# Kernel tuning notes

Hardware: AMD Instinct MI355X
Metric: run time of the kernel (lower is better)

## Reference

```python
import jax, jax.numpy as jnp
import numpy as np
from jax import lax


def setup_inputs() -> dict:
    key = jax.random.key(0)
    k1, k2 = jax.random.split(key)
    x = jax.random.normal(k1, (16, 256, 64, 64), dtype=jnp.float32)
    weight = jax.random.normal(k2, (1024, 256), dtype=jnp.float32)  # codebook (K, C)
    return {"x": x, "weight": weight}


def reference(x, weight):
    B, C, H, W = x.shape
    # (b c h w) -> (b h w) c
    xf = jnp.transpose(x, (0, 2, 3, 1)).reshape(-1, C)  # [N, C]
    d = (jnp.sum(xf * xf, axis=1, keepdims=True)
         + jnp.sum(weight * weight, axis=1)
         - 2.0 * (xf @ weight.T))
    indices = jnp.argmin(d, axis=1)  # [N], int
    z = weight[indices]  # [N, C] embedding lookup
    codebook_loss = jnp.mean((z - lax.stop_gradient(xf)) ** 2)
    commitment_loss = jnp.mean((xf - lax.stop_gradient(z)) ** 2)
    # straight-through estimator
    zq = xf + lax.stop_gradient(z - xf)
    zq = zq.reshape(B, H, W, C).transpose(0, 3, 1, 2)  # back to [B, C, H, W]
    sequence = indices.reshape(B, H, W)
    return zq, sequence, codebook_loss, commitment_loss
```

## Files before the change

### kernel.cpp

```cpp
#include <hip/hip_runtime.h>
#include <cfloat>

#define B_   16
#define C_   256
#define K_   1024
#define HW_  4096
#define N_   (B_ * HW_)
#define CHW_ (C_ * HW_)

#define SEQ_OFF  (B_ * C_ * HW_)
#define LOSS_OFF (SEQ_OFF + N_)

#define WT_F    0
#define WN_F    262144
#define WHB_F   263168
#define WLB_F   394240
#define RLIST_F 525312
#define RCNT_F  590848

#define EPS_GAP 0.03125f

typedef short bf16x8 __attribute__((ext_vector_type(8)));
typedef float f32x4  __attribute__((ext_vector_type(4)));

__device__ __forceinline__ unsigned short bf16_rne(float f) {
    unsigned u = __float_as_uint(f);
    unsigned r = u + 0x7fffu + ((u >> 16) & 1u);
    return (unsigned short)(r >> 16);
}
__device__ __forceinline__ float bf16_to_f(unsigned short h) {
    return __uint_as_float(((unsigned)h) << 16);
}
__device__ __forceinline__ int swz16k(int o) {
    return o ^ (((o >> 9) & 7) << 4);
}

__global__ __launch_bounds__(256) void transpose_w_kernel(
    const float* __restrict__ w, float* __restrict__ w_t)
{
    const int tid = blockIdx.x * 256 + threadIdx.x;
    const float4 v = reinterpret_cast<const float4*>(w)[tid];
    const int k = tid >> 6;
    const int c = (tid & 63) * 4;
    w_t[(size_t)(c + 0) * K_ + k] = v.x;
    w_t[(size_t)(c + 1) * K_ + k] = v.y;
    w_t[(size_t)(c + 2) * K_ + k] = v.z;
    w_t[(size_t)(c + 3) * K_ + k] = v.w;
}

__global__ __launch_bounds__(256) void wnorm_kernel(
    const float* __restrict__ w, float* __restrict__ wn)
{
    const int k = blockIdx.x * 256 + threadIdx.x;
    const float4* wr = reinterpret_cast<const float4*>(w + (size_t)k * C_);
    float s = 0.f;
#pragma unroll 8
    for (int c4 = 0; c4 < C_ / 4; ++c4) {
        const float4 v = wr[c4];
        s += v.x * v.x + v.y * v.y + v.z * v.z + v.w * v.w;
    }
    wn[k] = s;
}

__global__ __launch_bounds__(256) void wsplit_kernel(
    const float* __restrict__ w, unsigned short* __restrict__ whb,
    unsigned short* __restrict__ wlb)
{
    const int tid = blockIdx.x * 256 + threadIdx.x;
#pragma unroll
    for (int q = 0; q < 4; ++q) {
        const int i = tid * 4 + q;
        const float v = w[i];
        const unsigned short hi = bf16_rne(v);
        whb[i] = hi;
        wlb[i] = bf16_rne(v - bf16_to_f(hi));
    }
}

__global__ __launch_bounds__(512, 2) void argmin_mfma_kernel(
    const float* __restrict__ x, const unsigned short* __restrict__ whb,
    const unsigned short* __restrict__ wlb, const float* __restrict__ wnorm,
    float* __restrict__ seq, int* __restrict__ rlist, int* __restrict__ rcount)
{
    __shared__ __align__(16) char lds[65536];
    const int t  = threadIdx.x;
    const int l  = t & 63;
    const int wv = t >> 6;
    const int nb = blockIdx.x;
    const int b  = nb >> 4;
    const int hw0 = (nb & 15) << 8;
    const float* xb = x + (size_t)b * CHW_ + hw0;

    const int lr = l & 15;
    const int g  = l >> 4;

    bf16x8 ah[2][8], al[2][8];
    {
        float* xs = (float*)lds;
#pragma unroll
        for (int cc = 0; cc < 8; ++cc) {
#pragma unroll
            for (int q = 0; q < 4; ++q) {
                const int fi = t + q * 512;
                const int cl = fi >> 6;
                const int r4 = (fi & 63) << 2;
                const float4 v = *reinterpret_cast<const float4*>(
                    xb + (size_t)(cc * 32 + cl) * HW_ + r4);
                *reinterpret_cast<float4*>(xs + cl * 272 + r4) = v;
            }
            __syncthreads();
#pragma unroll
            for (int mt = 0; mt < 2; ++mt) {
                const int row = wv * 32 + mt * 16 + lr;
                bf16x8 vh, vl;
#pragma unroll
                for (int j = 0; j < 8; ++j) {
                    const float v = xs[(g * 8 + j) * 272 + row];
                    const unsigned short hi = bf16_rne(v);
                    vh[j] = (short)hi;
                    vl[j] = (short)bf16_rne(v - bf16_to_f(hi));
                }
                ah[mt][cc] = vh;
                al[mt][cc] = vl;
            }
            __syncthreads();
        }
    }

    char* const buf0 = lds;
    char* const buf1 = lds + 32768;
    const char* whbB = (const char*)whb;
    const char* wlbB = (const char*)wlb;

#define STAGE_CHUNK(ch, dst)                                                        \
    {                                                                               \
        const size_t goff = (size_t)(ch) * 16384;                                   \
        _Pragma("unroll")                                                           \
        for (int rr = 0; rr < 4; ++rr) {                                            \
            const int sIdx = wv * 4 + rr;                                           \
            const int region = sIdx >> 4;                                           \
            const int L = (sIdx & 15) * 1024;                                       \
            const int sw = swz16k(L + l * 16);                                      \
            const char* gp = (region ? wlbB : whbB) + goff + sw;                    \
            char* lp = (dst) + region * 16384 + L;                                  \
            __builtin_amdgcn_global_load_lds(                                       \
                (const __attribute__((address_space(1))) void*)gp,                  \
                (__attribute__((address_space(3))) void*)lp, 16, 0, 0);             \
        }                                                                           \
    }

    STAGE_CHUNK(0, buf0);
    __syncthreads();

    float m1v[2][4], m2v[2][4];
    int   i1v[2][4];
#pragma unroll
    for (int mt = 0; mt < 2; ++mt)
#pragma unroll
        for (int i = 0; i < 4; ++i) { m1v[mt][i] = FLT_MAX; m2v[mt][i] = FLT_MAX; i1v[mt][i] = 0; }

    int cur = 0;
    for (int ch = 0; ch < 32; ++ch) {
        char* const curbuf = cur ? buf1 : buf0;
        if (ch < 31) { STAGE_CHUNK(ch + 1, cur ? buf0 : buf1); }
        const int k0 = ch * 32;
        const float wn0 = wnorm[k0 + lr];
        const float wn1 = wnorm[k0 + 16 + lr];

        f32x4 acc[2][2];
#pragma unroll
        for (int mt = 0; mt < 2; ++mt)
#pragma unroll
            for (int nt = 0; nt < 2; ++nt) acc[mt][nt] = (f32x4){0.f, 0.f, 0.f, 0.f};

        const char* whs = curbuf;
        const char* wls = curbuf + 16384;
#pragma unroll
        for (int nt = 0; nt < 2; ++nt) {
#pragma unroll
            for (int s = 0; s < 8; ++s) {
                const int E = (nt * 16 + lr) * 512 + s * 64 + g * 16;
                const int sw = swz16k(E);
                const bf16x8 bh = *reinterpret_cast<const bf16x8*>(whs + sw);
                const bf16x8 bl = *reinterpret_cast<const bf16x8*>(wls + sw);
                acc[0][nt] = __builtin_amdgcn_mfma_f32_16x16x32_bf16(ah[0][s], bh, acc[0][nt], 0, 0, 0);
                acc[1][nt] = __builtin_amdgcn_mfma_f32_16x16x32_bf16(ah[1][s], bh, acc[1][nt], 0, 0, 0);
                acc[0][nt] = __builtin_amdgcn_mfma_f32_16x16x32_bf16(al[0][s], bh, acc[0][nt], 0, 0, 0);
                acc[1][nt] = __builtin_amdgcn_mfma_f32_16x16x32_bf16(al[1][s], bh, acc[1][nt], 0, 0, 0);
                acc[0][nt] = __builtin_amdgcn_mfma_f32_16x16x32_bf16(ah[0][s], bl, acc[0][nt], 0, 0, 0);
                acc[1][nt] = __builtin_amdgcn_mfma_f32_16x16x32_bf16(ah[1][s], bl, acc[1][nt], 0, 0, 0);
            }
        }

#pragma unroll
        for (int mt = 0; mt < 2; ++mt) {
#pragma unroll
            for (int nt = 0; nt < 2; ++nt) {
                const float wn = nt ? wn1 : wn0;
                const int k = k0 + nt * 16 + lr;
#pragma unroll
                for (int i = 0; i < 4; ++i) {
                    const float d = fmaf(-2.f, acc[mt][nt][i], wn);
                    const bool lt = d < m1v[mt][i];
                    const float nm2 = lt ? m1v[mt][i] : fminf(m2v[mt][i], d);
                    i1v[mt][i] = lt ? k : i1v[mt][i];
                    m1v[mt][i] = lt ? d : m1v[mt][i];
                    m2v[mt][i] = nm2;
                }
            }
        }
        __syncthreads();
        cur ^= 1;
    }
#undef STAGE_CHUNK

#pragma unroll
    for (int mask = 1; mask <= 8; mask <<= 1) {
#pragma unroll
        for (int mt = 0; mt < 2; ++mt) {
#pragma unroll
            for (int i = 0; i < 4; ++i) {
                const float om1 = __shfl_xor(m1v[mt][i], mask, 64);
                const int   oi1 = __shfl_xor(i1v[mt][i], mask, 64);
                const float om2 = __shfl_xor(m2v[mt][i], mask, 64);
                const bool lt = om1 < m1v[mt][i];
                const float nm2 = lt ? fminf(m1v[mt][i], om2) : fminf(m2v[mt][i], om1);
                i1v[mt][i] = lt ? oi1 : i1v[mt][i];
                m1v[mt][i] = lt ? om1 : m1v[mt][i];
                m2v[mt][i] = nm2;
            }
        }
    }

    if (lr == 0) {
#pragma unroll
        for (int mt = 0; mt < 2; ++mt) {
#pragma unroll
            for (int i = 0; i < 4; ++i) {
                const int m = mt * 16 + g * 4 + i;
                const int n = b * HW_ + hw0 + wv * 32 + m;
                seq[n] = (float)i1v[mt][i];
                if (m2v[mt][i] - m1v[mt][i] < EPS_GAP) {
                    const int pos = atomicAdd(rcount, 1);
                    rlist[pos] = n;
                }
            }
        }
    }
}

__global__ __launch_bounds__(256) void rescue_kernel(
    const float* __restrict__ x, const float* __restrict__ w_t,
    const float* __restrict__ wnorm, const int* __restrict__ rlist,
    const int* __restrict__ rcount, float* __restrict__ seq)
{
    __shared__ float xr[C_];
    __shared__ float bvs[4];
    __shared__ int   bis[4];
    const int t = threadIdx.x;
    const int cnt = *rcount;
    for (int ii = blockIdx.x; ii < cnt; ii += gridDim.x) {
        const int n = rlist[ii];
        const int b = n >> 12, hw = n & 4095;
        xr[t] = x[(size_t)b * CHW_ + (size_t)t * HW_ + hw];
        __syncthreads();
        float best = FLT_MAX; int bidx = 0;
#pragma unroll
        for (int q = 0; q < 4; ++q) {
            const int k = t + q * 256;
            float acc = 0.f;
            for (int c = 0; c < C_; ++c) acc = fmaf(xr[c], w_t[(size_t)c * K_ + k], acc);
            const float d = wnorm[k] - 2.f * acc;
            if (d < best || (d == best && k < bidx)) { best = d; bidx = k; }
        }
#pragma unroll
        for (int mask = 1; mask < 64; mask <<= 1) {
            const float ov = __shfl_xor(best, mask, 64);
            const int   oi = __shfl_xor(bidx, mask, 64);
            if (ov < best || (ov == best && oi < bidx)) { best = ov; bidx = oi; }
        }
        if ((t & 63) == 0) { bvs[t >> 6] = best; bis[t >> 6] = bidx; }
        __syncthreads();
        if (t == 0) {
            float bv = bvs[0]; int bi = bis[0];
#pragma unroll
            for (int w2 = 1; w2 < 4; ++w2)
                if (bvs[w2] < bv || (bvs[w2] == bv && bis[w2] < bi)) { bv = bvs[w2]; bi = bis[w2]; }
            seq[n] = (float)bi;
        }
        __syncthreads();
    }
}

__global__ __launch_bounds__(256) void gather_kernel(
    const float* __restrict__ x, const float* __restrict__ w,
    const float* __restrict__ seqf, float* __restrict__ zq,
    double* __restrict__ loss_acc)
{
    const int t   = threadIdx.x;
    const int nb  = blockIdx.x;
    const int b   = nb >> 6;
    const int hw0 = (nb & 63) << 6;
    const int r   = t & 63;
    const int cg  = t >> 6;
    const float* xb = x  + (size_t)b * CHW_ + hw0;
    float*       zb = zq + (size_t)b * CHW_ + hw0;
    const int idx = (int)seqf[b * HW_ + hw0 + r];
    const float* wrow = w + (size_t)idx * C_;

    float lsum = 0.f;
#pragma unroll 4
    for (int cc = 0; cc < 64; ++cc) {
        const int c = cg * 64 + cc;
        const float xv = xb[(size_t)c * HW_ + r];
        const float d  = wrow[c] - xv;
        zb[(size_t)c * HW_ + r] = xv + d;
        lsum += d * d;
    }
#pragma unroll
    for (int off = 32; off >= 1; off >>= 1) lsum += __shfl_down(lsum, off, 64);
    __shared__ float wsum[4];
    if ((t & 63) == 0) wsum[t >> 6] = lsum;
    __syncthreads();
    if (t == 0)
        atomicAdd(loss_acc, (double)(wsum[0] + wsum[1] + wsum[2] + wsum[3]));
}

__global__ void finalize_kernel(const double* __restrict__ acc, float* __restrict__ loss_out)
{
    const double s = *acc;
    const float m = (float)(s / (double)((size_t)N_ * C_));
    loss_out[0] = m;
    loss_out[1] = m;
}

extern "C" void kernel_launch(void* const* d_in, const int* in_sizes, int n_in,
                              void* d_out, int out_size, void* d_ws, size_t ws_size,
                              hipStream_t stream)
{
    (void)in_sizes; (void)n_in; (void)out_size; (void)d_ws; (void)ws_size;
    const float* x = (const float*)d_in[0];
    const float* w = (const float*)d_in[1];
    float* out = (float*)d_out;

    float*          w_t    = out + WT_F;
    float*          wn     = out + WN_F;
    unsigned short* whb    = (unsigned short*)(out + WHB_F);
    unsigned short* wlb    = (unsigned short*)(out + WLB_F);
    int*            rlist  = (int*)(out + RLIST_F);
    int*            rcount = (int*)(out + RCNT_F);
    float*          seq    = out + SEQ_OFF;
    double*         loss_acc = (double*)(out + LOSS_OFF);

    transpose_w_kernel<<<256, 256, 0, stream>>>(w, w_t);
    wnorm_kernel<<<4, 256, 0, stream>>>(w, wn);
    wsplit_kernel<<<256, 256, 0, stream>>>(w, whb, wlb);
    hipMemsetAsync((void*)rcount, 0, 4, stream);
    argmin_mfma_kernel<<<256, 512, 0, stream>>>(x, whb, wlb, wn, seq, rlist, rcount);
    rescue_kernel<<<1024, 256, 0, stream>>>(x, w_t, wn, rlist, rcount, seq);
    hipMemsetAsync((char*)d_out + (size_t)LOSS_OFF * 4, 0, 8, stream);
    gather_kernel<<<1024, 256, 0, stream>>>(x, w, seq, out, loss_acc);
    finalize_kernel<<<1, 1, 0, stream>>>(loss_acc, out + LOSS_OFF);
}
```

Baseline: 194.4 us.

## Switch argmin GEMM to 32x32x16 MFMA with pre-fragmented codebook layout

Replaces the 16x16x32 bf16 MFMA tiling with 32x32x16 MFMA, giving each wave 32 rows against 32 codes per chunk. The codebook split kernel now writes hi/lo bf16 parts directly in MFMA fragment order, so LDS staging becomes contiguous copies and the swizzle is dropped. Blocks shrink to 256 threads covering 128 positions with twice as many blocks, and the cross-lane reduction gains an index tie-break. The aim is fewer MFMA issues and simpler LDS addressing, at the cost of larger accumulator register use and possible LDS bank conflicts from the unswizzled reads.

After: 195.0 us. About the same (+0.3%).

```diff
diff --git a/kernel.cpp b/kernel.cpp
--- a/kernel.cpp
+++ b/kernel.cpp
@@ -21,7 +21,7 @@
 #define EPS_GAP 0.03125f
 
 typedef short bf16x8 __attribute__((ext_vector_type(8)));
-typedef float f32x4  __attribute__((ext_vector_type(4)));
+typedef float f32x16 __attribute__((ext_vector_type(16)));
 
 __device__ __forceinline__ unsigned short bf16_rne(float f) {
     unsigned u = __float_as_uint(f);
@@ -30,9 +30,6 @@
 }
 __device__ __forceinline__ float bf16_to_f(unsigned short h) {
     return __uint_as_float(((unsigned)h) << 16);
-}
-__device__ __forceinline__ int swz16k(int o) {
-    return o ^ (((o >> 9) & 7) << 4);
 }
 
 __global__ __launch_bounds__(256) void transpose_w_kernel(
@@ -62,22 +59,27 @@
     wn[k] = s;
 }
 
-__global__ __launch_bounds__(256) void wsplit_kernel(
+__global__ __launch_bounds__(256) void wsplit_frag_kernel(
     const float* __restrict__ w, unsigned short* __restrict__ whb,
     unsigned short* __restrict__ wlb)
 {
     const int tid = blockIdx.x * 256 + threadIdx.x;
-#pragma unroll
-    for (int q = 0; q < 4; ++q) {
-        const int i = tid * 4 + q;
-        const float v = w[i];
-        const unsigned short hi = bf16_rne(v);
-        whb[i] = hi;
-        wlb[i] = bf16_rne(v - bf16_to_f(hi));
-    }
-}
-
-__global__ __launch_bounds__(512, 2) void argmin_mfma_kernel(
+    const int k  = tid >> 5;
+    const int c8 = tid & 31;
+    const float* src = w + (size_t)k * C_ + c8 * 8;
+    unsigned short h[8], lo[8];
+#pragma unroll
+    for (int j = 0; j < 8; ++j) {
+        const float v = src[j];
+        h[j] = bf16_rne(v);
+        lo[j] = bf16_rne(v - bf16_to_f(h[j]));
+    }
+    const size_t dst = (size_t)(k >> 5) * 8192 + (size_t)c8 * 256 + (size_t)(k & 31) * 8;
+#pragma unroll
+    for (int j = 0; j < 8; ++j) { whb[dst + j] = h[j]; wlb[dst + j] = lo[j]; }
+}
+
+__global__ __launch_bounds__(256, 2) void argmin_mfma_kernel(
     const float* __restrict__ x, const unsigned short* __restrict__ whb,
     const unsigned short* __restrict__ wlb, const float* __restrict__ wnorm,
     float* __restrict__ seq, int* __restrict__ rlist, int* __restrict__ rcount)
@@ -87,41 +89,42 @@
     const int l  = t & 63;
     const int wv = t >> 6;
     const int nb = blockIdx.x;
-    const int b  = nb >> 4;
-    const int hw0 = (nb & 15) << 8;
+    const int b  = nb >> 5;
+    const int hw0 = (nb & 31) << 7;
     const float* xb = x + (size_t)b * CHW_ + hw0;
 
-    const int lr = l & 15;
-    const int g  = l >> 4;
-
-    bf16x8 ah[2][8], al[2][8];
+    const int col   = l & 31;
+    const int khalf = l >> 5;
+
+    bf16x8 ah[16], al[16];
     {
         float* xs = (float*)lds;
 #pragma unroll
         for (int cc = 0; cc < 8; ++cc) {
 #pragma unroll
             for (int q = 0; q < 4; ++q) {
-                const int fi = t + q * 512;
-                const int cl = fi >> 6;
-                const int r4 = (fi & 63) << 2;
+                const int fi = q * 256 + t;
+                const int cl = fi >> 5;
+                const int r4 = (fi & 31) << 2;
                 const float4 v = *reinterpret_cast<const float4*>(
                     xb + (size_t)(cc * 32 + cl) * HW_ + r4);
-                *reinterpret_cast<float4*>(xs + cl * 272 + r4) = v;
+                *reinterpret_cast<float4*>(xs + cl * 132 + r4) = v;
             }
             __syncthreads();
-#pragma unroll
-            for (int mt = 0; mt < 2; ++mt) {
-                const int row = wv * 32 + mt * 16 + lr;
+            const int row = wv * 32 + col;
+#pragma unroll
+            for (int h = 0; h < 2; ++h) {
+                const int ks = cc * 2 + h;
                 bf16x8 vh, vl;
 #pragma unroll
                 for (int j = 0; j < 8; ++j) {
-                    const float v = xs[(g * 8 + j) * 272 + row];
+                    const float v = xs[(h * 16 + khalf * 8 + j) * 132 + row];
                     const unsigned short hi = bf16_rne(v);
                     vh[j] = (short)hi;
                     vl[j] = (short)bf16_rne(v - bf16_to_f(hi));
                 }
-                ah[mt][cc] = vh;
-                al[mt][cc] = vl;
+                ah[ks] = vh;
+                al[ks] = vl;
             }
             __syncthreads();
         }
@@ -134,116 +137,89 @@
 
 #define STAGE_CHUNK(ch, dst)                                                        \
     {                                                                               \
-        const size_t goff = (size_t)(ch) * 16384;                                   \
+        const size_t goff = (size_t)(ch) * 16384 + (size_t)(wv * 4) * 1024;         \
+        const int    loff = wv * 4 * 1024;                                          \
         _Pragma("unroll")                                                           \
         for (int rr = 0; rr < 4; ++rr) {                                            \
-            const int sIdx = wv * 4 + rr;                                           \
-            const int region = sIdx >> 4;                                           \
-            const int L = (sIdx & 15) * 1024;                                       \
-            const int sw = swz16k(L + l * 16);                                      \
-            const char* gp = (region ? wlbB : whbB) + goff + sw;                    \
-            char* lp = (dst) + region * 16384 + L;                                  \
             __builtin_amdgcn_global_load_lds(                                       \
-                (const __attribute__((address_space(1))) void*)gp,                  \
-                (__attribute__((address_space(3))) void*)lp, 16, 0, 0);             \
+                (const __attribute__((address_space(1))) void*)                    \
+                    (whbB + goff + rr * 1024 + l * 16),                             \
+                (__attribute__((address_space(3))) void*)                           \
+                    ((dst) + loff + rr * 1024), 16, 0, 0);                          \
+            __builtin_amdgcn_global_load_lds(                                       \
+                (const __attribute__((address_space(1))) void*)                    \
+                    (wlbB + goff + rr * 1024 + l * 16),                             \
+                (__attribute__((address_space(3))) void*)                           \
+                    ((dst) + 16384 + loff + rr * 1024), 16, 0, 0);                  \
         }                                                                           \
     }
 
     STAGE_CHUNK(0, buf0);
     __syncthreads();
 
-    float m1v[2][4], m2v[2][4];
-    int   i1v[2][4];
-#pragma unroll
-    for (int mt = 0; mt < 2; ++mt)
-#pragma unroll
-        for (int i = 0; i < 4; ++i) { m1v[mt][i] = FLT_MAX; m2v[mt][i] = FLT_MAX; i1v[mt][i] = 0; }
-
-    int cur = 0;
+    float m1v[16], m2v[16];
+    int   i1v[16];
+#pragma unroll
+    for (int r = 0; r < 16; ++r) { m1v[r] = FLT_MAX; m2v[r] = FLT_MAX; i1v[r] = 0; }
+
     for (int ch = 0; ch < 32; ++ch) {
-        char* const curbuf = cur ? buf1 : buf0;
-        if (ch < 31) { STAGE_CHUNK(ch + 1, cur ? buf0 : buf1); }
+        char* const curbuf = (ch & 1) ? buf1 : buf0;
+        if (ch < 31) { STAGE_CHUNK(ch + 1, (ch & 1) ? buf0 : buf1); }
         const int k0 = ch * 32;
-        const float wn0 = wnorm[k0 + lr];
-        const float wn1 = wnorm[k0 + 16 + lr];
-
-        f32x4 acc[2][2];
-#pragma unroll
-        for (int mt = 0; mt < 2; ++mt)
-#pragma unroll
-            for (int nt = 0; nt < 2; ++nt) acc[mt][nt] = (f32x4){0.f, 0.f, 0.f, 0.f};
-
-        const char* whs = curbuf;
-        const char* wls = curbuf + 16384;
-#pragma unroll
-        for (int nt = 0; nt < 2; ++nt) {
-#pragma unroll
-            for (int s = 0; s < 8; ++s) {
-                const int E = (nt * 16 + lr) * 512 + s * 64 + g * 16;
-                const int sw = swz16k(E);
-                const bf16x8 bh = *reinterpret_cast<const bf16x8*>(whs + sw);
-                const bf16x8 bl = *reinterpret_cast<const bf16x8*>(wls + sw);
-                acc[0][nt] = __builtin_amdgcn_mfma_f32_16x16x32_bf16(ah[0][s], bh, acc[0][nt], 0, 0, 0);
-                acc[1][nt] = __builtin_amdgcn_mfma_f32_16x16x32_bf16(ah[1][s], bh, acc[1][nt], 0, 0, 0);
-                acc[0][nt] = __builtin_amdgcn_mfma_f32_16x16x32_bf16(al[0][s], bh, acc[0][nt], 0, 0, 0);
-                acc[1][nt] = __builtin_amdgcn_mfma_f32_16x16x32_bf16(al[1][s], bh, acc[1][nt], 0, 0, 0);
-                acc[0][nt] = __builtin_amdgcn_mfma_f32_16x16x32_bf16(ah[0][s], bl, acc[0][nt], 0, 0, 0);
-                acc[1][nt] = __builtin_amdgcn_mfma_f32_16x16x32_bf16(ah[1][s], bl, acc[1][nt], 0, 0, 0);
-            }
-        }
-
-#pragma unroll
-        for (int mt = 0; mt < 2; ++mt) {
-#pragma unroll
-            for (int nt = 0; nt < 2; ++nt) {
-                const float wn = nt ? wn1 : wn0;
-                const int k = k0 + nt * 16 + lr;
-#pragma unroll
-                for (int i = 0; i < 4; ++i) {
-                    const float d = fmaf(-2.f, acc[mt][nt][i], wn);
-                    const bool lt = d < m1v[mt][i];
-                    const float nm2 = lt ? m1v[mt][i] : fminf(m2v[mt][i], d);
-                    i1v[mt][i] = lt ? k : i1v[mt][i];
-                    m1v[mt][i] = lt ? d : m1v[mt][i];
-                    m2v[mt][i] = nm2;
-                }
-            }
+        const float wnc = wnorm[k0 + col];
+
+        f32x16 accA = {0.f}, accB = {0.f};
+#pragma unroll
+        for (int r = 0; r < 16; ++r) { accA[r] = 0.f; accB[r] = 0.f; }
+
+        const char* hb = curbuf;
+        const char* lb = curbuf + 16384;
+#pragma unroll
+        for (int ks = 0; ks < 16; ++ks) {
+            const bf16x8 bh = *reinterpret_cast<const bf16x8*>(hb + ks * 1024 + (l << 4));
+            const bf16x8 bl = *reinterpret_cast<const bf16x8*>(lb + ks * 1024 + (l << 4));
+            accA = __builtin_amdgcn_mfma_f32_32x32x16_bf16(ah[ks], bh, accA, 0, 0, 0);
+            accB = __builtin_amdgcn_mfma_f32_32x32x16_bf16(al[ks], bh, accB, 0, 0, 0);
+            accA = __builtin_amdgcn_mfma_f32_32x32x16_bf16(ah[ks], bl, accA, 0, 0, 0);
+        }
+
+        const int kidx = k0 + col;
+#pragma unroll
+        for (int r = 0; r < 16; ++r) {
+            const float d = fmaf(-2.f, accA[r] + accB[r], wnc);
+            const bool lt = d < m1v[r];
+            m2v[r] = lt ? m1v[r] : fminf(m2v[r], d);
+            i1v[r] = lt ? kidx : i1v[r];
+            m1v[r] = lt ? d : m1v[r];
         }
         __syncthreads();
-        cur ^= 1;
     }
 #undef STAGE_CHUNK
 
 #pragma unroll
-    for (int mask = 1; mask <= 8; mask <<= 1) {
-#pragma unroll
-        for (int mt = 0; mt < 2; ++mt) {
-#pragma unroll
-            for (int i = 0; i < 4; ++i) {
-                const float om1 = __shfl_xor(m1v[mt][i], mask, 64);
-                const int   oi1 = __shfl_xor(i1v[mt][i], mask, 64);
-                const float om2 = __shfl_xor(m2v[mt][i], mask, 64);
-                const bool lt = om1 < m1v[mt][i];
-                const float nm2 = lt ? fminf(m1v[mt][i], om2) : fminf(m2v[mt][i], om1);
-                i1v[mt][i] = lt ? oi1 : i1v[mt][i];
-                m1v[mt][i] = lt ? om1 : m1v[mt][i];
-                m2v[mt][i] = nm2;
-            }
-        }
-    }
-
-    if (lr == 0) {
-#pragma unroll
-        for (int mt = 0; mt < 2; ++mt) {
-#pragma unroll
-            for (int i = 0; i < 4; ++i) {
-                const int m = mt * 16 + g * 4 + i;
-                const int n = b * HW_ + hw0 + wv * 32 + m;
-                seq[n] = (float)i1v[mt][i];
-                if (m2v[mt][i] - m1v[mt][i] < EPS_GAP) {
-                    const int pos = atomicAdd(rcount, 1);
-                    rlist[pos] = n;
-                }
+    for (int mask = 1; mask <= 16; mask <<= 1) {
+#pragma unroll
+        for (int r = 0; r < 16; ++r) {
+            const float om1 = __shfl_xor(m1v[r], mask, 64);
+            const int   oi1 = __shfl_xor(i1v[r], mask, 64);
+            const float om2 = __shfl_xor(m2v[r], mask, 64);
+            const bool lt = om1 < m1v[r] || (om1 == m1v[r] && oi1 < i1v[r]);
+            const float nm2 = lt ? fminf(m1v[r], om2) : fminf(m2v[r], om1);
+            i1v[r] = lt ? oi1 : i1v[r];
+            m1v[r] = lt ? om1 : m1v[r];
+            m2v[r] = nm2;
+        }
+    }
+
+    if (col == 0) {
+#pragma unroll
+        for (int r = 0; r < 16; ++r) {
+            const int row_local = (r & 3) + 8 * (r >> 2) + 4 * khalf;
+            const int n = b * HW_ + hw0 + wv * 32 + row_local;
+            seq[n] = (float)i1v[r];
+            if (m2v[r] - m1v[r] < EPS_GAP) {
+                const int pos = atomicAdd(rcount, 1);
+                rlist[pos] = n;
             }
         }
     }
@@ -354,9 +330,9 @@
 
     transpose_w_kernel<<<256, 256, 0, stream>>>(w, w_t);
     wnorm_kernel<<<4, 256, 0, stream>>>(w, wn);
-    wsplit_kernel<<<256, 256, 0, stream>>>(w, whb, wlb);
+    wsplit_frag_kernel<<<128, 256, 0, stream>>>(w, whb, wlb);
     hipMemsetAsync((void*)rcount, 0, 4, stream);
-    argmin_mfma_kernel<<<256, 512, 0, stream>>>(x, whb, wlb, wn, seq, rlist, rcount);
+    argmin_mfma_kernel<<<512, 256, 0, stream>>>(x, whb, wlb, wn, seq, rlist, rcount);
     rescue_kernel<<<1024, 256, 0, stream>>>(x, w_t, wn, rlist, rcount, seq);
     hipMemsetAsync((char*)d_out + (size_t)LOSS_OFF * 4, 0, 8, stream);
     gather_kernel<<<1024, 256, 0, stream>>>(x, w, seq, out, loss_acc);
```
